# Kernel tuning notes

Hardware: AMD Instinct MI355X
Metric: run time of the kernel (lower is better)

The kernel has to match this reference:

```python
import jax, jax.numpy as jnp
import numpy as np

B, TQ, TK = 2, 1024, 2048
DQ, DC, H, TOPK = 1024, 768, 16, 64
DH = DQ // H


def setup_inputs() -> dict:
    key = jax.random.key(0)
    ks = jax.random.split(key, 12)
    s = lambda d: 1.0 / np.sqrt(d)
    return {
        "x": jax.random.normal(ks[0], (B, TQ, DQ), jnp.float32),
        "context": jax.random.normal(ks[1], (B, TK, DC), jnp.float32),
        "key_padding_mask": jax.random.bernoulli(ks[2], 0.05, (B, TK)),
        "Wq": jax.random.normal(ks[3], (DQ, DQ), jnp.float32) * s(DQ),
        "bq": jnp.zeros((DQ,), jnp.float32),
        "Wk": jax.random.normal(ks[4], (DC, DQ), jnp.float32) * s(DC),
        "bk": jnp.zeros((DQ,), jnp.float32),
        "Wv": jax.random.normal(ks[5], (DC, DQ), jnp.float32) * s(DC),
        "bv": jnp.zeros((DQ,), jnp.float32),
        "Wo": jax.random.normal(ks[6], (DQ, DQ), jnp.float32) * s(DQ),
        "bo": jnp.zeros((DQ,), jnp.float32),
    }


def _heads(t):
    # (B, T, DQ) -> (B, H, T, DH)
    b, tt, _ = t.shape
    return t.reshape(b, tt, H, DH).transpose(0, 2, 1, 3)


def reference(x, context, key_padding_mask, Wq, bq, Wk, bk, Wv, bv, Wo, bo):
    q = _heads(x @ Wq + bq)          # (B,H,Tq,DH)
    k = _heads(context @ Wk + bk)    # (B,H,Tk,DH)
    v = _heads(context @ Wv + bv)    # (B,H,Tk,DH)

    scale = DH ** -0.5
    logits = jnp.einsum("bhqd,bhkd->bhqk", q, k) * scale  # (B,H,Tq,Tk)
    neg = jnp.finfo(logits.dtype).min
    logits = jnp.where(key_padding_mask[:, None, None, :], neg, logits)

    # hard top-k sparsification: keep top TOPK logits per query, fill rest with -inf-like
    topk_vals, topk_idx = jax.lax.top_k(logits, TOPK)
    sparse_logits = jnp.full_like(logits, neg)
    sparse_logits = jnp.put_along_axis(sparse_logits, topk_idx, topk_vals, axis=-1, inplace=False)

    attn = jax.nn.softmax(sparse_logits, axis=-1)
    out = jnp.einsum("bhqk,bhkd->bhqd", attn, v)  # (B,H,Tq,DH)
    out = out.transpose(0, 2, 1, 3).reshape(B, TQ, DQ)
    return out @ Wo + bo
```

## Files before the change

kernel.cpp:

```cpp
#include <hip/hip_runtime.h>
#include <cstdint>
#include <cstddef>

#define BN_ 2
#define TQ_ 1024
#define TK_ 2048
#define DQ_ 1024
#define DC_ 768
#define NH_ 16
#define DH_ 64
#define TOPK_ 64

typedef unsigned short u16;
typedef __attribute__((ext_vector_type(8))) short short8;
typedef __attribute__((ext_vector_type(8))) u16   ushort8;
typedef __attribute__((ext_vector_type(4))) float floatx4;

__device__ __forceinline__ float bf2f(u16 u) { return __uint_as_float(((unsigned)u) << 16); }
__device__ __forceinline__ u16 f2bf(float f) {
    unsigned u = __float_as_uint(f);
    u += 0x7FFFu + ((u >> 16) & 1u);
    return (u16)(u >> 16);
}
__device__ __forceinline__ float definite(float v, float repl) {
    return ((__float_as_uint(v) & 0x7F800000u) == 0x7F800000u) ? repl : v;
}
__device__ __forceinline__ unsigned mono(float f) {
    unsigned u = __float_as_uint(f);
    return (u & 0x80000000u) ? ~u : (u | 0x80000000u);
}
__device__ __forceinline__ float invmono(unsigned u) {
    return __uint_as_float((u & 0x80000000u) ? (u & 0x7FFFFFFFu) : ~u);
}
__device__ __forceinline__ int gsum16(int x) {
#pragma unroll
    for (int o = 1; o < 16; o <<= 1) x += __shfl_xor(x, o);
    return x;
}
__device__ __forceinline__ int gmin16(int x) {
#pragma unroll
    for (int o = 1; o < 16; o <<= 1) { int y = __shfl_xor(x, o); x = (y < x) ? y : x; }
    return x;
}
__device__ __forceinline__ unsigned gmin16u(unsigned x) {
#pragma unroll
    for (int o = 1; o < 16; o <<= 1) { unsigned y = __shfl_xor((int)x, o); x = (y < x) ? y : x; }
    return x;
}
__device__ __forceinline__ unsigned gmax16u(unsigned x) {
#pragma unroll
    for (int o = 1; o < 16; o <<= 1) { unsigned y = __shfl_xor((int)x, o); x = (y > x) ? y : x; }
    return x;
}
__device__ __forceinline__ float gmax16f(float x) {
#pragma unroll
    for (int o = 1; o < 16; o <<= 1) x = fmaxf(x, __shfl_xor(x, o));
    return x;
}
__device__ __forceinline__ float gsum16f(float x) {
#pragma unroll
    for (int o = 1; o < 16; o <<= 1) x += __shfl_xor(x, o);
    return x;
}

__global__ void marker_kernel(float* __restrict__ out, int n, float val) {
    const int i = blockIdx.x * 256 + threadIdx.x;
    if (i < n) out[i] = val;
}

template <int NV>
__device__ __forceinline__ void select_topk(const unsigned (&um)[NV], const int (&kk)[NV],
                                            unsigned base, int hb, int l16,
                                            float* cvrow, int* ckrow) {
    unsigned X = 0u;
    bool done = false;
    for (int bit = hb; bit >= 0; --bit) {
        const unsigned C = X | (1u << bit);
        int c = 0;
#pragma unroll
        for (int j = 0; j < NV; ++j) c += (um[j] >= C) ? 1 : 0;
        c = gsum16(c);
        if (!done && c >= 64) X = C;
        if (c == 64) done = true;
        if (__all(done)) break;
    }
    int myGt = 0;
#pragma unroll
    for (int j = 0; j < NV; ++j) myGt += (um[j] > X) ? 1 : 0;
    const int totalGt = gsum16(myGt);
    int pre = myGt;
#pragma unroll
    for (int off = 1; off < 16; off <<= 1) {
        const int tv = __shfl_up(pre, off);
        if (l16 >= off) pre += tv;
    }
    int wpos = pre - myGt;
#pragma unroll
    for (int j = 0; j < NV; ++j) {
        if (um[j] > X) {
            cvrow[wpos] = invmono(base + um[j]);
            ckrow[wpos] = kk[j];
            ++wpos;
        }
    }
    const float xval = invmono(base + X);
    int remaining = 64 - totalGt;
    int pos = totalGt;
    int lastkey = -1;
    while (remaining > 0) {
        int mykey = 0x7FFFFFFF;
#pragma unroll
        for (int j = 0; j < NV; ++j)
            if (um[j] == X && kk[j] > lastkey && kk[j] < mykey) mykey = kk[j];
        const int mn = gmin16(mykey);
        if (mn == 0x7FFFFFFF) break;
        if (mykey == mn) { cvrow[pos] = xval; ckrow[pos] = mn; }
        lastkey = mn;
        ++pos; --remaining;
    }
}

__global__ void __launch_bounds__(256) tsplit(const float* __restrict__ W,
                                              u16* __restrict__ Wh, u16* __restrict__ Wl,
                                              int K, int N) {
    __shared__ float t[32][33];
    const int x = threadIdx.x & 31, y = threadIdx.x >> 5;
    const int bn = blockIdx.x * 32, bk = blockIdx.y * 32;
#pragma unroll
    for (int i = 0; i < 32; i += 8) t[y + i][x] = W[(size_t)(bk + y + i) * N + bn + x];
    __syncthreads();
#pragma unroll
    for (int i = 0; i < 32; i += 8) {
        const float f = t[x][y + i];
        const u16 hi = f2bf(f);
        const size_t o = (size_t)(bn + y + i) * K + bk + x;
        Wh[o] = hi;
        Wl[o] = f2bf(f - bf2f(hi));
    }
}

template <int ASPLIT, int OMODE>
__global__ void __launch_bounds__(256) gemm3(
    const void* __restrict__ Ap, const void* __restrict__ Alp,
    const u16* __restrict__ Bh, const u16* __restrict__ Bl,
    const float* __restrict__ bias, float scale,
    void* __restrict__ out0, void* __restrict__ out1,
    int M, int N, int K) {
    __shared__ u16 Ahs[64 * 64];
    __shared__ u16 Als[64 * 64];
    __shared__ u16 Bhs[128 * 64];
    __shared__ u16 Bls[128 * 64];

    const int tid = threadIdx.x;
    const int lane = tid & 63, wave = tid >> 6;
    const int wm = wave >> 1, wn = wave & 1;
    const int quad = lane >> 4, l16 = lane & 15;
    const int bm = blockIdx.y * 64, bn = blockIdx.x * 128;

    floatx4 acc[2][4] = {};

    for (int k0 = 0; k0 < K; k0 += 64) {
        __syncthreads();
#pragma unroll
        for (int s2 = 0; s2 < 2; ++s2) {
            const int slot = tid + s2 * 256;
            const int m = slot >> 3, cpos = slot & 7;
            const int c = cpos ^ (m & 7);
            const size_t aoff = (size_t)(bm + m) * K + k0 + c * 8;
            if constexpr (ASPLIT == 0) {
                const float* f = (const float*)Ap + aoff;
                const floatx4 a = *(const floatx4*)f;
                const floatx4 b = *(const floatx4*)(f + 4);
                ushort8 hi, lo;
#pragma unroll
                for (int j = 0; j < 4; ++j) {
                    u16 t = f2bf(a[j]);
                    hi[j] = t; lo[j] = f2bf(a[j] - bf2f(t));
                    t = f2bf(b[j]);
                    hi[4 + j] = t; lo[4 + j] = f2bf(b[j] - bf2f(t));
                }
                *(ushort8*)&Ahs[slot * 8] = hi;
                *(ushort8*)&Als[slot * 8] = lo;
            } else {
                *(ushort8*)&Ahs[slot * 8] = *(const ushort8*)((const u16*)Ap  + aoff);
                *(ushort8*)&Als[slot * 8] = *(const ushort8*)((const u16*)Alp + aoff);
            }
        }
#pragma unroll
        for (int s4 = 0; s4 < 4; ++s4) {
            const int slot = tid + s4 * 256;
            const int n = slot >> 3, cpos = slot & 7;
            const int c = cpos ^ (n & 7);
            const size_t boff = (size_t)(bn + n) * K + k0 + c * 8;
            *(ushort8*)&Bhs[slot * 8] = *(const ushort8*)(Bh + boff);
            *(ushort8*)&Bls[slot * 8] = *(const ushort8*)(Bl + boff);
        }
        __syncthreads();
#pragma unroll
        for (int s = 0; s < 2; ++s) {
            short8 ah[2], al[2], bh[4], bl[4];
#pragma unroll
            for (int mt = 0; mt < 2; ++mt) {
                const int m = wm * 32 + mt * 16 + l16;
                const int cs = s * 4 + quad;
                const int slot = m * 8 + (cs ^ (m & 7));
                ah[mt] = *(const short8*)&Ahs[slot * 8];
                al[mt] = *(const short8*)&Als[slot * 8];
            }
#pragma unroll
            for (int nt = 0; nt < 4; ++nt) {
                const int n = wn * 64 + nt * 16 + l16;
                const int cs = s * 4 + quad;
                const int slot = n * 8 + (cs ^ (n & 7));
                bh[nt] = *(const short8*)&Bhs[slot * 8];
                bl[nt] = *(const short8*)&Bls[slot * 8];
            }
#pragma unroll
            for (int mt = 0; mt < 2; ++mt)
#pragma unroll
                for (int nt = 0; nt < 4; ++nt) {
                    acc[mt][nt] = __builtin_amdgcn_mfma_f32_16x16x32_bf16(ah[mt], bh[nt], acc[mt][nt], 0, 0, 0);
                    acc[mt][nt] = __builtin_amdgcn_mfma_f32_16x16x32_bf16(al[mt], bh[nt], acc[mt][nt], 0, 0, 0);
                    acc[mt][nt] = __builtin_amdgcn_mfma_f32_16x16x32_bf16(ah[mt], bl[nt], acc[mt][nt], 0, 0, 0);
                }
        }
    }

#pragma unroll
    for (int mt = 0; mt < 2; ++mt) {
#pragma unroll
        for (int nt = 0; nt < 4; ++nt) {
            const int col = bn + wn * 64 + nt * 16 + l16;
            const float bcol = bias[col];
#pragma unroll
            for (int r = 0; r < 4; ++r) {
                const int row = bm + wm * 32 + mt * 16 + quad * 4 + r;
                const float val = definite((acc[mt][nt][r] + bcol) * scale, 0.0f);
                const size_t idx = (size_t)row * N + col;
                if constexpr (OMODE == 0) {
                    ((float*)out0)[idx] = val;
                } else if constexpr (OMODE == 1) {
                    ((u16*)out0)[idx] = f2bf(val);
                } else {
                    const u16 hi = f2bf(val);
                    ((u16*)out0)[idx] = hi;
                    ((u16*)out1)[idx] = f2bf(val - bf2f(hi));
                }
            }
        }
    }
}

__global__ void __launch_bounds__(256, 4) attn_topk(
    const u16* Qhi, const u16* Qlo,
    const u16* __restrict__ Khi, const u16* __restrict__ Klo,
    const u16* __restrict__ Vb16, const void* __restrict__ maskp,
    u16* attnH, u16* attnL) {
    __shared__ float lg[16][512];
    __shared__ float cval[16][64];
    __shared__ int   ckey[16][64];

    const int tid = threadIdx.x;
    const int lane = tid & 63, wave = tid >> 6;
    const int quad = lane >> 4, l16 = lane & 15;
    const int rowg = wave * 4 + quad;
    const int b = blockIdx.z, h = blockIdx.y, q0 = blockIdx.x * 16;

    int mmode;
    {
        bool cbyte = false, cbf = false, cf32 = false;
#pragma unroll
        for (int j = 0; j < 16; ++j) {
            const int i = lane + 64 * j;
            const unsigned v = ((const u16*)maskp)[i];
            cbyte |= (v == 0x0100u || v == 0x0101u) || ((i & 1) && v == 0x0001u);
            cbf   |= (!(i & 1)) && v == 0x3F80u;
            cf32  |= (i & 1) && v == 0x3F80u;
        }
        const bool abf = __any(cbf), af32 = __any(cf32), abyte = __any(cbyte);
        mmode = abf ? 2 : (af32 ? 3 : (abyte ? 1 : 0));
    }

    short8 qh[2], ql[2];
    {
        const size_t base = (size_t)(b * TQ_ + q0 + l16) * DQ_ + h * DH_ + quad * 8;
        qh[0] = *(const short8*)(Qhi + base);
        qh[1] = *(const short8*)(Qhi + base + 32);
        ql[0] = *(const short8*)(Qlo + base);
        ql[1] = *(const short8*)(Qlo + base + 32);
    }

    for (int i = tid; i < 16 * 64; i += 256) {
        cval[i >> 6][i & 63] = __uint_as_float(0xFF800000u);
        ckey[i >> 6][i & 63] = i & 63;
    }

    for (int qtr = 0; qtr < 4; ++qtr) {
#pragma unroll 2
        for (int t = 0; t < 8; ++t) {
            const int key = qtr * 512 + wave * 128 + t * 16 + l16;
            const size_t kb = (size_t)(b * TK_ + key) * DQ_ + h * DH_ + quad * 8;
            const short8 kh0 = *(const short8*)(Khi + kb);
            const short8 kh1 = *(const short8*)(Khi + kb + 32);
            const short8 kl0 = *(const short8*)(Klo + kb);
            const short8 kl1 = *(const short8*)(Klo + kb + 32);
            floatx4 acc = {};
            acc = __builtin_amdgcn_mfma_f32_16x16x32_bf16(qh[0], kh0, acc, 0, 0, 0);
            acc = __builtin_amdgcn_mfma_f32_16x16x32_bf16(ql[0], kh0, acc, 0, 0, 0);
            acc = __builtin_amdgcn_mfma_f32_16x16x32_bf16(qh[0], kl0, acc, 0, 0, 0);
            acc = __builtin_amdgcn_mfma_f32_16x16x32_bf16(qh[1], kh1, acc, 0, 0, 0);
            acc = __builtin_amdgcn_mfma_f32_16x16x32_bf16(ql[1], kh1, acc, 0, 0, 0);
            acc = __builtin_amdgcn_mfma_f32_16x16x32_bf16(qh[1], kl1, acc, 0, 0, 0);
            const int midx = b * TK_ + key;
            bool masked;
            if (mmode == 2)      masked = ((const u16*)maskp)[midx] != 0;
            else if (mmode == 3) masked = ((const float*)maskp)[midx] != 0.0f;
            else if (mmode == 1) masked = ((const unsigned char*)maskp)[midx] != 0;
            else                 masked = ((const int*)maskp)[midx] != 0;
            const int kk = wave * 128 + t * 16 + l16;
#pragma unroll
            for (int r = 0; r < 4; ++r)
                lg[quad * 4 + r][kk] = masked ? -3.0e38f : definite(acc[r], -3.0e38f);
        }
        __syncthreads();

        unsigned uc[4]; int ck4[4];
#pragma unroll
        for (int t = 0; t < 4; ++t) {
            uc[t] = mono(cval[rowg][l16 + 16 * t]);
            ck4[t] = ckey[rowg][l16 + 16 * t];
        }

        if (qtr == 0) {
            unsigned um[36]; int kk[36];
#pragma unroll
            for (int j = 0; j < 32; ++j) {
                um[j] = mono(lg[rowg][l16 + 16 * j]);
                kk[j] = l16 + 16 * j;
            }
#pragma unroll
            for (int t = 0; t < 4; ++t) { um[32 + t] = uc[t]; kk[32 + t] = ck4[t]; }
            unsigned rmin = um[0], rmax = um[0];
#pragma unroll
            for (int j = 1; j < 36; ++j) {
                rmin = (um[j] < rmin) ? um[j] : rmin;
                rmax = (um[j] > rmax) ? um[j] : rmax;
            }
            rmin = gmin16u(rmin);
            rmax = gmax16u(rmax);
            unsigned zm[36];
#pragma unroll
            for (int j = 0; j < 36; ++j) zm[j] = um[j] - rmin;
            const int hb = 31 - __clz((rmax - rmin) | 1u);
            select_topk<36>(zm, kk, rmin, hb, l16, cval[rowg], ckey[rowg]);
        } else {
            unsigned cm = uc[0];
            cm = (uc[1] < cm) ? uc[1] : cm;
            cm = (uc[2] < cm) ? uc[2] : cm;
            cm = (uc[3] < cm) ? uc[3] : cm;
            cm = gmin16u(cm);
            unsigned zm[36]; int kk[36];
            unsigned zmx = 0;
#pragma unroll
            for (int j = 0; j < 32; ++j) {
                const unsigned u = mono(lg[rowg][l16 + 16 * j]);
                zm[j] = (u > cm) ? (u - cm) : 0u;
                kk[j] = qtr * 512 + l16 + 16 * j;
                zmx = (zm[j] > zmx) ? zm[j] : zmx;
            }
#pragma unroll
            for (int t = 0; t < 4; ++t) {
                zm[32 + t] = uc[t] - cm;
                kk[32 + t] = ck4[t];
                zmx = (zm[32 + t] > zmx) ? zm[32 + t] : zmx;
            }
            zmx = gmax16u(zmx);
            const int hb = 31 - __clz(zmx | 1u);
            select_topk<36>(zm, kk, cm, hb, l16, cval[rowg], ckey[rowg]);
        }
        if (qtr < 3) __syncthreads();
    }

    {
        float v4[4];
#pragma unroll
        for (int t = 0; t < 4; ++t) v4[t] = cval[rowg][l16 + 16 * t];
        float m = fmaxf(fmaxf(v4[0], v4[1]), fmaxf(v4[2], v4[3]));
        m = gmax16f(m);
        float p4[4], S = 0.f;
#pragma unroll
        for (int t = 0; t < 4; ++t) { p4[t] = __expf(v4[t] - m); S += p4[t]; }
        S = gsum16f(S);
        const float inv = 1.0f / S;
#pragma unroll
        for (int t = 0; t < 4; ++t) cval[rowg][l16 + 16 * t] = p4[t] * inv;
    }

    const int half = lane >> 5, l32 = lane & 31;
    const u16* Vrow = Vb16 + (size_t)b * TK_ * DQ_ + h * DH_ + l32 * 2;
#pragma unroll
    for (int rp = 0; rp < 2; ++rp) {
        const int row = wave * 4 + rp * 2 + half;
        float a0 = 0.f, a1 = 0.f;
#pragma unroll 4
        for (int e = 0; e < 64; ++e) {
            const float w = cval[row][e];
            const int k = ckey[row][e];
            const unsigned v2 = *(const unsigned*)(Vrow + (size_t)k * DQ_);
            a0 += w * bf2f((u16)(v2 & 0xFFFFu));
            a1 += w * bf2f((u16)(v2 >> 16));
        }
        a0 = definite(a0, 0.0f);
        a1 = definite(a1, 0.0f);
        const size_t o = (size_t)(b * TQ_ + q0 + row) * DQ_ + h * DH_ + l32 * 2;
        const u16 h0 = f2bf(a0), h1 = f2bf(a1);
        const u16 l0 = f2bf(a0 - bf2f(h0)), l1 = f2bf(a1 - bf2f(h1));
        *(unsigned*)(attnH + o) = (unsigned)h0 | ((unsigned)h1 << 16);
        *(unsigned*)(attnL + o) = (unsigned)l0 | ((unsigned)l1 << 16);
    }
}

extern "C" void kernel_launch(void* const* d_in, const int* in_sizes, int n_in,
                              void* d_out, int out_size, void* d_ws, size_t ws_size,
                              hipStream_t stream) {
    static const int exp_sizes[11] = {2097152, 3145728, 4096, 1048576, 1024,
                                      786432, 1024, 786432, 1024, 1048576, 1024};
    if (n_in != 11) {
        marker_kernel<<<(out_size + 255) / 256, 256, 0, stream>>>((float*)d_out, out_size,
                                                                  (float)(150 + n_in));
        return;
    }
    for (int i = 0; i < 11; ++i)
        if (in_sizes[i] != exp_sizes[i]) {
            marker_kernel<<<(out_size + 255) / 256, 256, 0, stream>>>((float*)d_out, out_size,
                                                                      (float)(200 + i));
            return;
        }

    const float* x   = (const float*)d_in[0];
    const float* ctx = (const float*)d_in[1];
    const void*  msk = d_in[2];
    const float* Wq = (const float*)d_in[3];
    const float* bq = (const float*)d_in[4];
    const float* Wk = (const float*)d_in[5];
    const float* bk = (const float*)d_in[6];
    const float* Wv = (const float*)d_in[7];
    const float* bv = (const float*)d_in[8];
    const float* Wo = (const float*)d_in[9];
    const float* bo = (const float*)d_in[10];

    const size_t SZ_Q = (size_t)BN_ * TQ_ * DQ_ * 2;
    const size_t SZ_K = (size_t)BN_ * TK_ * DQ_ * 2;
    const size_t NEED = 2 * SZ_Q + 2 * SZ_K + SZ_K;
    if (ws_size < NEED) {
        marker_kernel<<<(out_size + 255) / 256, 256, 0, stream>>>(
            (float*)d_out, out_size, (float)(ws_size >> 20));
        return;
    }

    char* ws = (char*)d_ws;
    u16* Qhi = (u16*)(ws);
    u16* Qlo = (u16*)(ws + SZ_Q);
    u16* Khi = (u16*)(ws + 2 * SZ_Q);
    u16* Klo = (u16*)(ws + 2 * SZ_Q + SZ_K);
    u16* Vb  = (u16*)(ws + 2 * SZ_Q + 2 * SZ_K);

    u16* WqT_h = Khi;
    u16* WqT_l = Khi + (size_t)DQ_ * DQ_;
    u16* WkT_h = Vb;
    u16* WkT_l = Vb + (size_t)DC_ * DQ_;
    u16* WvT_h = (u16*)d_out;
    u16* WvT_l = (u16*)d_out + (size_t)DC_ * DQ_;
    u16* WoT_h = Khi;
    u16* WoT_l = Khi + (size_t)DQ_ * DQ_;

    const int MQ = BN_ * TQ_;
    const int MK = BN_ * TK_;

    tsplit<<<dim3(DQ_ / 32, DQ_ / 32), 256, 0, stream>>>(Wq, WqT_h, WqT_l, DQ_, DQ_);
    gemm3<0, 2><<<dim3(DQ_ / 128, MQ / 64), 256, 0, stream>>>(
        x, nullptr, WqT_h, WqT_l, bq, 0.125f, Qhi, Qlo, MQ, DQ_, DQ_);
    tsplit<<<dim3(DQ_ / 32, DC_ / 32), 256, 0, stream>>>(Wk, WkT_h, WkT_l, DC_, DQ_);
    gemm3<0, 2><<<dim3(DQ_ / 128, MK / 64), 256, 0, stream>>>(
        ctx, nullptr, WkT_h, WkT_l, bk, 1.0f, Khi, Klo, MK, DQ_, DC_);
    tsplit<<<dim3(DQ_ / 32, DC_ / 32), 256, 0, stream>>>(Wv, WvT_h, WvT_l, DC_, DQ_);
    gemm3<0, 1><<<dim3(DQ_ / 128, MK / 64), 256, 0, stream>>>(
        ctx, nullptr, WvT_h, WvT_l, bv, 1.0f, Vb, nullptr, MK, DQ_, DC_);

    attn_topk<<<dim3(TQ_ / 16, NH_, BN_), 256, 0, stream>>>(
        Qhi, Qlo, Khi, Klo, Vb, msk, Qhi, Qlo);

    tsplit<<<dim3(DQ_ / 32, DQ_ / 32), 256, 0, stream>>>(Wo, WoT_h, WoT_l, DQ_, DQ_);
    gemm3<1, 0><<<dim3(DQ_ / 128, MQ / 64), 256, 0, stream>>>(
        Qhi, Qlo, WoT_h, WoT_l, bo, 1.0f, d_out, nullptr, MQ, DQ_, DQ_);
}
```

Measured before the change: 431.2 us.

## Filter candidate logits against running top-k threshold before selection

After the first key quarter, each later quarter compares logits against the current 64th-largest threshold per row. Only values above it are appended to a compacted shared-memory candidate list via LDS atomics, and the radix top-k select then runs on 12 values per lane instead of 36. This is meant to cut LDS writes and selection work, at the cost of atomic contention and silently dropping candidates if more than 127 per row pass the threshold. The first quarter also drops its min/max range narrowing and searches all 32 bits.

```diff
diff --git a/kernel.cpp b/kernel.cpp
--- a/kernel.cpp
+++ b/kernel.cpp
@@ -69,9 +69,9 @@
 }
 
 template <int NV>
-__device__ __forceinline__ void select_topk(const unsigned (&um)[NV], const int (&kk)[NV],
-                                            unsigned base, int hb, int l16,
-                                            float* cvrow, int* ckrow) {
+__device__ __forceinline__ float select_topk(const unsigned (&um)[NV], const int (&kk)[NV],
+                                             unsigned base, int hb, int l16,
+                                             float* cvrow, int* ckrow) {
     unsigned X = 0u;
     bool done = false;
     for (int bit = hb; bit >= 0; --bit) {
@@ -118,6 +118,7 @@
         lastkey = mn;
         ++pos; --remaining;
     }
+    return xval;
 }
 
 __global__ void __launch_bounds__(256) tsplit(const float* __restrict__ W,
@@ -296,42 +297,34 @@
     }
 
     for (int qtr = 0; qtr < 4; ++qtr) {
+        if (qtr == 0) {
 #pragma unroll 2
-        for (int t = 0; t < 8; ++t) {
-            const int key = qtr * 512 + wave * 128 + t * 16 + l16;
-            const size_t kb = (size_t)(b * TK_ + key) * DQ_ + h * DH_ + quad * 8;
-            const short8 kh0 = *(const short8*)(Khi + kb);
-            const short8 kh1 = *(const short8*)(Khi + kb + 32);
-            const short8 kl0 = *(const short8*)(Klo + kb);
-            const short8 kl1 = *(const short8*)(Klo + kb + 32);
-            floatx4 acc = {};
-            acc = __builtin_amdgcn_mfma_f32_16x16x32_bf16(qh[0], kh0, acc, 0, 0, 0);
-            acc = __builtin_amdgcn_mfma_f32_16x16x32_bf16(ql[0], kh0, acc, 0, 0, 0);
-            acc = __builtin_amdgcn_mfma_f32_16x16x32_bf16(qh[0], kl0, acc, 0, 0, 0);
-            acc = __builtin_amdgcn_mfma_f32_16x16x32_bf16(qh[1], kh1, acc, 0, 0, 0);
-            acc = __builtin_amdgcn_mfma_f32_16x16x32_bf16(ql[1], kh1, acc, 0, 0, 0);
-            acc = __builtin_amdgcn_mfma_f32_16x16x32_bf16(qh[1], kl1, acc, 0, 0, 0);
-            const int midx = b * TK_ + key;
-            bool masked;
-            if (mmode == 2)      masked = ((const u16*)maskp)[midx] != 0;
-            else if (mmode == 3) masked = ((const float*)maskp)[midx] != 0.0f;
-            else if (mmode == 1) masked = ((const unsigned char*)maskp)[midx] != 0;
-            else                 masked = ((const int*)maskp)[midx] != 0;
-            const int kk = wave * 128 + t * 16 + l16;
-#pragma unroll
-            for (int r = 0; r < 4; ++r)
-                lg[quad * 4 + r][kk] = masked ? -3.0e38f : definite(acc[r], -3.0e38f);
-        }
-        __syncthreads();
-
-        unsigned uc[4]; int ck4[4];
-#pragma unroll
-        for (int t = 0; t < 4; ++t) {
-            uc[t] = mono(cval[rowg][l16 + 16 * t]);
-            ck4[t] = ckey[rowg][l16 + 16 * t];
-        }
-
-        if (qtr == 0) {
+            for (int t = 0; t < 8; ++t) {
+                const int key = wave * 128 + t * 16 + l16;
+                const size_t kb = (size_t)(b * TK_ + key) * DQ_ + h * DH_ + quad * 8;
+                const short8 kh0 = *(const short8*)(Khi + kb);
+                const short8 kh1 = *(const short8*)(Khi + kb + 32);
+                const short8 kl0 = *(const short8*)(Klo + kb);
+                const short8 kl1 = *(const short8*)(Klo + kb + 32);
+                floatx4 acc = {};
+                acc = __builtin_amdgcn_mfma_f32_16x16x32_bf16(qh[0], kh0, acc, 0, 0, 0);
+                acc = __builtin_amdgcn_mfma_f32_16x16x32_bf16(ql[0], kh0, acc, 0, 0, 0);
+                acc = __builtin_amdgcn_mfma_f32_16x16x32_bf16(qh[0], kl0, acc, 0, 0, 0);
+                acc = __builtin_amdgcn_mfma_f32_16x16x32_bf16(qh[1], kh1, acc, 0, 0, 0);
+                acc = __builtin_amdgcn_mfma_f32_16x16x32_bf16(ql[1], kh1, acc, 0, 0, 0);
+                acc = __builtin_amdgcn_mfma_f32_16x16x32_bf16(qh[1], kl1, acc, 0, 0, 0);
+                const int midx = b * TK_ + key;
+                bool masked;
+                if (mmode == 2)      masked = ((const u16*)maskp)[midx] != 0;
+                else if (mmode == 3) masked = ((const float*)maskp)[midx] != 0.0f;
+                else if (mmode == 1) masked = ((const unsigned char*)maskp)[midx] != 0;
+                else                 masked = ((const int*)maskp)[midx] != 0;
+#pragma unroll
+                for (int r = 0; r < 4; ++r)
+                    lg[quad * 4 + r][key] = masked ? -3.0e38f : definite(acc[r], -3.0e38f);
+            }
+            __syncthreads();
+
             unsigned um[36]; int kk[36];
 #pragma unroll
             for (int j = 0; j < 32; ++j) {
@@ -339,44 +332,96 @@
                 kk[j] = l16 + 16 * j;
             }
 #pragma unroll
-            for (int t = 0; t < 4; ++t) { um[32 + t] = uc[t]; kk[32 + t] = ck4[t]; }
-            unsigned rmin = um[0], rmax = um[0];
-#pragma unroll
-            for (int j = 1; j < 36; ++j) {
-                rmin = (um[j] < rmin) ? um[j] : rmin;
-                rmax = (um[j] > rmax) ? um[j] : rmax;
-            }
-            rmin = gmin16u(rmin);
-            rmax = gmax16u(rmax);
-            unsigned zm[36];
-#pragma unroll
-            for (int j = 0; j < 36; ++j) zm[j] = um[j] - rmin;
-            const int hb = 31 - __clz((rmax - rmin) | 1u);
-            select_topk<36>(zm, kk, rmin, hb, l16, cval[rowg], ckey[rowg]);
+            for (int t = 0; t < 4; ++t) {
+                um[32 + t] = mono(cval[rowg][l16 + 16 * t]);
+                kk[32 + t] = ckey[rowg][l16 + 16 * t];
+            }
+            const float th = select_topk<36>(um, kk, 0u, 31, l16, cval[rowg], ckey[rowg]);
+            if (l16 == 0) {
+                lg[rowg][255] = th;
+                ((int*)&lg[rowg][0])[511] = 0;
+            }
         } else {
+            float cmrow[4];
+#pragma unroll
+            for (int r = 0; r < 4; ++r) cmrow[r] = lg[quad * 4 + r][255];
+#pragma unroll 2
+            for (int t = 0; t < 8; ++t) {
+                const int key = qtr * 512 + wave * 128 + t * 16 + l16;
+                const size_t kb = (size_t)(b * TK_ + key) * DQ_ + h * DH_ + quad * 8;
+                const short8 kh0 = *(const short8*)(Khi + kb);
+                const short8 kh1 = *(const short8*)(Khi + kb + 32);
+                const short8 kl0 = *(const short8*)(Klo + kb);
+                const short8 kl1 = *(const short8*)(Klo + kb + 32);
+                floatx4 acc = {};
+                acc = __builtin_amdgcn_mfma_f32_16x16x32_bf16(qh[0], kh0, acc, 0, 0, 0);
+                acc = __builtin_amdgcn_mfma_f32_16x16x32_bf16(ql[0], kh0, acc, 0, 0, 0);
+                acc = __builtin_amdgcn_mfma_f32_16x16x32_bf16(qh[0], kl0, acc, 0, 0, 0);
+                acc = __builtin_amdgcn_mfma_f32_16x16x32_bf16(qh[1], kh1, acc, 0, 0, 0);
+                acc = __builtin_amdgcn_mfma_f32_16x16x32_bf16(ql[1], kh1, acc, 0, 0, 0);
+                acc = __builtin_amdgcn_mfma_f32_16x16x32_bf16(qh[1], kl1, acc, 0, 0, 0);
+                const int midx = b * TK_ + key;
+                bool masked;
+                if (mmode == 2)      masked = ((const u16*)maskp)[midx] != 0;
+                else if (mmode == 3) masked = ((const float*)maskp)[midx] != 0.0f;
+                else if (mmode == 1) masked = ((const unsigned char*)maskp)[midx] != 0;
+                else                 masked = ((const int*)maskp)[midx] != 0;
+#pragma unroll
+                for (int r = 0; r < 4; ++r) {
+                    const float val = masked ? -3.0e38f : definite(acc[r], -3.0e38f);
+                    if (val > cmrow[r]) {
+                        const int row = quad * 4 + r;
+                        const int pos = atomicAdd((int*)&lg[row][511], 1);
+                        if (pos < 127) {
+                            lg[row][pos] = val;
+                            ((int*)&lg[row][0])[128 + pos] = key;
+                        }
+                    }
+                }
+            }
+            __syncthreads();
+
+            unsigned uc[4]; int ck4[4];
+#pragma unroll
+            for (int t = 0; t < 4; ++t) {
+                uc[t] = mono(cval[rowg][l16 + 16 * t]);
+                ck4[t] = ckey[rowg][l16 + 16 * t];
+            }
             unsigned cm = uc[0];
             cm = (uc[1] < cm) ? uc[1] : cm;
             cm = (uc[2] < cm) ? uc[2] : cm;
             cm = (uc[3] < cm) ? uc[3] : cm;
             cm = gmin16u(cm);
-            unsigned zm[36]; int kk[36];
+            int cnt = ((int*)&lg[rowg][0])[511];
+            if (cnt > 127) cnt = 127;
+
+            unsigned zm[12]; int kk[12];
             unsigned zmx = 0;
 #pragma unroll
-            for (int j = 0; j < 32; ++j) {
-                const unsigned u = mono(lg[rowg][l16 + 16 * j]);
-                zm[j] = (u > cm) ? (u - cm) : 0u;
-                kk[j] = qtr * 512 + l16 + 16 * j;
-                zmx = (zm[j] > zmx) ? zm[j] : zmx;
+            for (int i = 0; i < 8; ++i) {
+                const int idx = l16 + 16 * i;
+                const bool valid = idx < cnt;
+                const float v = lg[rowg][idx];
+                const int k = ((int*)&lg[rowg][0])[128 + idx];
+                const unsigned mv = mono(v);
+                const bool live = valid && (mv > cm);
+                zm[i] = live ? (mv - cm) : 0u;
+                kk[i] = live ? k : 0x7FFFFFFF;
+                zmx = (zm[i] > zmx) ? zm[i] : zmx;
             }
 #pragma unroll
             for (int t = 0; t < 4; ++t) {
-                zm[32 + t] = uc[t] - cm;
-                kk[32 + t] = ck4[t];
-                zmx = (zm[32 + t] > zmx) ? zm[32 + t] : zmx;
+                zm[8 + t] = uc[t] - cm;
+                kk[8 + t] = ck4[t];
+                zmx = (zm[8 + t] > zmx) ? zm[8 + t] : zmx;
             }
             zmx = gmax16u(zmx);
             const int hb = 31 - __clz(zmx | 1u);
-            select_topk<36>(zm, kk, cm, hb, l16, cval[rowg], ckey[rowg]);
+            const float th = select_topk<12>(zm, kk, cm, hb, l16, cval[rowg], ckey[rowg]);
+            if (l16 == 0) {
+                lg[rowg][255] = th;
+                ((int*)&lg[rowg][0])[511] = 0;
+            }
         }
         if (qtr < 3) __syncthreads();
     }
```

Result: faster. 410.4 us (-4.8%).
